# Kernel tuning notes

Measured on AMD Instinct MI355X. Metric: run time of the kernel, lower is better.

Reference implementation:

```python
import jax, jax.numpy as jnp
import numpy as np

HEADS = 8
DIM_HEAD = 64
MAX_REL = 200  # max_rel_dist


def setup_inputs() -> dict:
    key = jax.random.key(0)
    ks = jax.random.split(key, 5)
    B, N, D = 4, 2048, 512
    x = jax.random.normal(ks[0], (B, N, D), dtype=jnp.float32)
    temporal_mask = jax.random.randint(ks[1], (N, N), 0, 2, dtype=jnp.int32)
    gamma = jnp.ones((D,), jnp.float32)
    beta = jnp.zeros((D,), jnp.float32)
    Wqkv = jax.random.normal(ks[2], (D, 3 * HEADS * DIM_HEAD), dtype=jnp.float32) * 0.02
    Wout = jax.random.normal(ks[3], (HEADS * DIM_HEAD, D), dtype=jnp.float32) * 0.02
    bout = jnp.zeros((D,), jnp.float32)
    rel_table = jax.random.normal(ks[4], (2 * MAX_REL - 1,), dtype=jnp.float32) * 0.02
    return {"x": x, "gamma": gamma, "beta": beta, "Wqkv": Wqkv, "Wout": Wout,
            "bout": bout, "rel_table": rel_table, "temporal_mask": temporal_mask}


def reference(x, gamma, beta, Wqkv, Wout, bout, rel_table, temporal_mask):
    B, N, D = x.shape
    scale = DIM_HEAD ** -0.5
    # LayerNorm
    mu = jnp.mean(x, axis=-1, keepdims=True)
    var = jnp.mean(jnp.square(x - mu), axis=-1, keepdims=True)
    xn = (x - mu) * jax.lax.rsqrt(var + 1e-5) * gamma + beta
    # QKV projection (no bias), split heads: b n (h d) -> b h n d
    qkv = xn @ Wqkv  # [B, N, 3*H*d]
    q, k, v = jnp.split(qkv, 3, axis=-1)
    split = lambda t: t.reshape(B, N, HEADS, DIM_HEAD).transpose(0, 2, 1, 3)
    q, k, v = split(q), split(k), split(v)
    # scores with learned relative-position bias
    dots = jnp.einsum('bhnd,bhmd->bhnm', q, k) * scale  # [B,H,N,N]
    idx = jnp.arange(N)
    rel = jnp.clip(idx[:, None] - idx[None, :], -(MAX_REL - 1), MAX_REL - 1) + MAX_REL - 1
    dots = dots + rel_table[rel][None, None, :, :]
    # temporal mask (0 -> -inf); large negative for grad safety
    dots = jnp.where(temporal_mask[None, None, :, :] == 0, jnp.float32(-1e9), dots)
    attn = jax.nn.softmax(dots, axis=-1)
    out = jnp.einsum('bhnm,bhmd->bhnd', attn, v)
    out = out.transpose(0, 2, 1, 3).reshape(B, N, HEADS * DIM_HEAD)
    return out @ Wout + bout
```

## Files before the change

kernel.cpp:

```cpp
#include <hip/hip_runtime.h>

typedef __attribute__((ext_vector_type(8))) short bf16x8;
typedef __attribute__((ext_vector_type(4))) short bf16x4;
typedef __attribute__((ext_vector_type(4))) float f32x4;
typedef unsigned short ushort_t;

#define B_ 4
#define H_ 8
#define N_ 2048
#define D_ 512
#define MAXREL 199
#define LOG2E 1.4426950408889634f

__device__ __forceinline__ ushort_t f2bf(float f) {
    union { float f; unsigned u; } v; v.f = f;
    unsigned r = v.u + 0x7fffu + ((v.u >> 16) & 1u);
    return (ushort_t)(r >> 16);
}
__device__ __forceinline__ float bf2f(ushort_t u) {
    union { unsigned u; float f; } v; v.u = ((unsigned)u) << 16;
    return v.f;
}
__device__ __forceinline__ float fexp2(float x) {
#if __has_builtin(__builtin_amdgcn_exp2f)
    return __builtin_amdgcn_exp2f(x);
#else
    return __expf(x * 0.6931471805599453f);
#endif
}
__device__ __forceinline__ unsigned cvt_pk_bf16(float lo, float hi) {
    unsigned r;
    asm("v_cvt_pk_bf16_f32 %0, %1, %2" : "=v"(r) : "v"(lo), "v"(hi));
    return r;
}
__device__ __forceinline__ void gl_lds16(const ushort_t* g, ushort_t* l) {
    __builtin_amdgcn_global_load_lds(
        (const __attribute__((address_space(1))) void*)g,
        (__attribute__((address_space(3))) void*)l,
        16, 0, 0);
}

#define PREP_LN    2048
#define PREP_WQ    768
#define PREP_WO    256
__global__ __launch_bounds__(256) void prep_kernel(const float* __restrict__ x,
                                                   const float* __restrict__ gamma,
                                                   const float* __restrict__ beta,
                                                   ushort_t* __restrict__ xn,
                                                   const float* __restrict__ Wqkv,
                                                   ushort_t* __restrict__ WqkvT,
                                                   const float* __restrict__ Wout,
                                                   ushort_t* __restrict__ WoutT) {
    __shared__ float smem[32 * 33];
    const int blk = blockIdx.x;
    const int t = threadIdx.x;

    if (blk < PREP_LN) {
        const int row = blk * 4 + (t >> 6);
        const int l = t & 63;
        const float* xr = x + (size_t)row * D_;
        float4 a = *(const float4*)&xr[l * 4];
        float4 c = *(const float4*)&xr[256 + l * 4];
        float s = (a.x + a.y) + (a.z + a.w) + (c.x + c.y) + (c.z + c.w);
        #pragma unroll
        for (int o = 1; o < 64; o <<= 1) s += __shfl_xor(s, o);
        float mu = s * (1.0f / D_);
        float dx0 = a.x - mu, dx1 = a.y - mu, dx2 = a.z - mu, dx3 = a.w - mu;
        float dy0 = c.x - mu, dy1 = c.y - mu, dy2 = c.z - mu, dy3 = c.w - mu;
        float s2 = dx0*dx0 + dx1*dx1 + dx2*dx2 + dx3*dx3
                 + dy0*dy0 + dy1*dy1 + dy2*dy2 + dy3*dy3;
        #pragma unroll
        for (int o = 1; o < 64; o <<= 1) s2 += __shfl_xor(s2, o);
        float rs = rsqrtf(s2 * (1.0f / D_) + 1e-5f);
        float4 g1 = *(const float4*)&gamma[l * 4];
        float4 g2 = *(const float4*)&gamma[256 + l * 4];
        float4 b1 = *(const float4*)&beta[l * 4];
        float4 b2 = *(const float4*)&beta[256 + l * 4];
        ushort_t* yr = xn + (size_t)row * D_;
        union { ushort_t us[4]; unsigned long long ll; } o1, o2;
        o1.us[0] = f2bf(dx0 * rs * g1.x + b1.x);
        o1.us[1] = f2bf(dx1 * rs * g1.y + b1.y);
        o1.us[2] = f2bf(dx2 * rs * g1.z + b1.z);
        o1.us[3] = f2bf(dx3 * rs * g1.w + b1.w);
        o2.us[0] = f2bf(dy0 * rs * g2.x + b2.x);
        o2.us[1] = f2bf(dy1 * rs * g2.y + b2.y);
        o2.us[2] = f2bf(dy2 * rs * g2.z + b2.z);
        o2.us[3] = f2bf(dy3 * rs * g2.w + b2.w);
        *(unsigned long long*)(yr + l * 4) = o1.ll;
        *(unsigned long long*)(yr + 256 + l * 4) = o2.ll;
    } else {
        const float* W; ushort_t* Wt; int Nn, i;
        if (blk < PREP_LN + PREP_WQ) {
            i = blk - PREP_LN; W = Wqkv; Wt = WqkvT; Nn = 1536;
        } else {
            i = blk - (PREP_LN + PREP_WQ); W = Wout; Wt = WoutT; Nn = 512;
        }
        const int nb = Nn >> 5;
        const int bx = (i % nb) * 32, by = (i / nb) * 32;
        const int tx = t & 31, ty = t >> 5;
        float (*tile)[33] = (float(*)[33])smem;
        #pragma unroll
        for (int k = 0; k < 32; k += 8)
            tile[ty + k][tx] = W[(size_t)(by + ty + k) * Nn + bx + tx];
        __syncthreads();
        #pragma unroll
        for (int k = 0; k < 32; k += 8)
            Wt[(size_t)(bx + ty + k) * 512 + by + tx] = f2bf(tile[tx][ty + k]);
    }
}

#define QKV_BIAS_BLKS 512
__global__ __launch_bounds__(256) void gemm_qkv(const ushort_t* __restrict__ A,
                                                const ushort_t* __restrict__ Bt,
                                                ushort_t* __restrict__ qb,
                                                ushort_t* __restrict__ kb,
                                                ushort_t* __restrict__ vb,
                                                const float* __restrict__ rel,
                                                const int* __restrict__ mask,
                                                ushort_t* __restrict__ bp) {
    const int bid = blockIdx.x;
    const int t = threadIdx.x;

    if (bid < QKV_BIAS_BLKS) {
        const int base = bid * 8192;
        #pragma unroll
        for (int p = 0; p < 8; p++) {
            int idx = base + p * 1024 + t * 4;
            int n = idx >> 11, m = idx & 2047;
            const int4 mv = *(const int4*)&mask[idx];
            union { ushort_t us[4]; unsigned long long ll; } pkv;
            #pragma unroll
            for (int j = 0; j < 4; j++) {
                int dl = n - (m + j);
                dl = dl < -MAXREL ? -MAXREL : (dl > MAXREL ? MAXREL : dl);
                int mj = (j == 0) ? mv.x : (j == 1) ? mv.y : (j == 2) ? mv.z : mv.w;
                float v = (mj == 0) ? -1e9f : rel[dl + MAXREL] * LOG2E;
                pkv.us[j] = f2bf(v);
            }
            int off = ((n >> 7) << 18) + ((m >> 6) << 13) + (((n >> 4) & 7) << 10)
                    + (((m >> 4) & 3) << 8) + (((m >> 2) & 3) << 6) + ((n & 15) << 2);
            *(unsigned long long*)(bp + off) = pkv.ll;
        }
        return;
    }

    __shared__ ushort_t As[2][4096];
    __shared__ ushort_t Bs[2][4096];
    const int gid = bid - QKV_BIAS_BLKS;
    const int lane = t & 63, w = t >> 6;
    const int m16 = lane & 15, quad = lane >> 4;
    const int wr = w >> 1, wc = w & 1;
    const int r0 = (gid / 12) * 128, c0 = (gid % 12) * 128;

    const ushort_t* Ag = A  + (size_t)(r0 + (t >> 2)) * D_ + (t & 3) * 8;
    const ushort_t* Bg = Bt + (size_t)(c0 + (t >> 2)) * D_ + (t & 3) * 8;

    f32x4 acc[4][4];
    #pragma unroll
    for (int i = 0; i < 4; i++)
        #pragma unroll
        for (int j = 0; j < 4; j++) acc[i][j] = (f32x4){0.f, 0.f, 0.f, 0.f};

    {
        ushort_t* AsW = As[0] + w * 512;
        ushort_t* BsW = Bs[0] + w * 512;
        gl_lds16(Ag, AsW);
        gl_lds16(Ag + (size_t)64 * D_, AsW + 2048);
        gl_lds16(Bg, BsW);
        gl_lds16(Bg + (size_t)64 * D_, BsW + 2048);
    }
    __syncthreads();

    for (int k0 = 0; k0 < D_; k0 += 32) {
        const int buf = (k0 >> 5) & 1;
        if (k0 + 32 < D_) {
            ushort_t* AsW = As[buf ^ 1] + w * 512;
            ushort_t* BsW = Bs[buf ^ 1] + w * 512;
            gl_lds16(Ag + k0 + 32, AsW);
            gl_lds16(Ag + k0 + 32 + (size_t)64 * D_, AsW + 2048);
            gl_lds16(Bg + k0 + 32, BsW);
            gl_lds16(Bg + k0 + 32 + (size_t)64 * D_, BsW + 2048);
        }
        bf16x8 af[4], bfr[4];
        #pragma unroll
        for (int rt = 0; rt < 4; rt++)
            af[rt] = *(const bf16x8*)(As[buf] + (wr * 64 + rt * 16 + m16) * 32 + quad * 8);
        #pragma unroll
        for (int ct = 0; ct < 4; ct++)
            bfr[ct] = *(const bf16x8*)(Bs[buf] + (wc * 64 + ct * 16 + m16) * 32 + quad * 8);
        #pragma unroll
        for (int rt = 0; rt < 4; rt++)
            #pragma unroll
            for (int ct = 0; ct < 4; ct++)
                acc[rt][ct] = __builtin_amdgcn_mfma_f32_16x16x32_bf16(af[rt], bfr[ct], acc[rt][ct], 0, 0, 0);
        __syncthreads();
    }

    const int b_blk = r0 >> 11, n_base = r0 & 2047;
    if ((c0 >> 9) == 2) {
        ushort_t* SH = As[0];
        #pragma unroll
        for (int ph = 0; ph < 2; ph++) {
            if (ph) __syncthreads();
            if (wc == ph) {
                #pragma unroll
                for (int ct = 0; ct < 4; ct++) {
                    int dcol = ct * 16 + m16;
                    #pragma unroll
                    for (int rt = 0; rt < 4; rt++) {
                        int nl = wr * 64 + rt * 16 + quad * 4;
                        union { ushort_t us[4]; unsigned long long ll; } pkv;
                        #pragma unroll
                        for (int r = 0; r < 4; r++) pkv.us[r] = f2bf(acc[rt][ct][r]);
                        *(unsigned long long*)(&SH[dcol * 128 + (nl ^ ((dcol & 7) << 3))]) = pkv.ll;
                    }
                }
            }
            __syncthreads();
            int h = ((c0 + ph * 64) >> 6) & 7;
            #pragma unroll
            for (int p = 0; p < 4; p++) {
                int dr = p * 16 + (t >> 4);
                int n0 = (t & 15) * 8;
                bf16x8 vv = *(const bf16x8*)&SH[dr * 128 + (n0 ^ ((dr & 7) << 3))];
                *(bf16x8*)(vb + ((size_t)(b_blk * H_ + h) * 64 + dr) * N_ + n_base + n0) = vv;
            }
        }
    } else {
        #pragma unroll
        for (int ct = 0; ct < 4; ct++) {
            int cc = c0 + wc * 64 + ct * 16;
            int which = cc >> 9;
            int h = (cc >> 6) & 7;
            int d = (cc & 63) + m16;
            #pragma unroll
            for (int rt = 0; rt < 4; rt++) {
                int rowb = r0 + wr * 64 + rt * 16 + quad * 4;
                int b = rowb >> 11, n0 = rowb & 2047;
                if (which == 0) {
                    #pragma unroll
                    for (int r = 0; r < 4; r++)
                        qb[((size_t)((b * H_ + h) * N_ + n0 + r)) * 64 + d] = f2bf(acc[rt][ct][r] * (0.125f * LOG2E));
                } else {
                    #pragma unroll
                    for (int r = 0; r < 4; r++)
                        kb[((size_t)((b * H_ + h) * N_ + n0 + r)) * 64 + d] = f2bf(acc[rt][ct][r]);
                }
            }
        }
    }
}

__global__ __launch_bounds__(256) void gemm_out(const ushort_t* __restrict__ A,
                                                const ushort_t* __restrict__ Bt,
                                                const float* __restrict__ bias,
                                                float* __restrict__ C) {
    __shared__ ushort_t As[2][2048];
    __shared__ ushort_t Bs[2][4096];
    const int t = threadIdx.x;
    const int lane = t & 63, w = t >> 6;
    const int m16 = lane & 15, quad = lane >> 4;
    const int wr = w >> 1, wc = w & 1;
    const int r0 = blockIdx.y * 64, c0 = blockIdx.x * 128;

    const ushort_t* Ag = A  + (size_t)(r0 + (t >> 2)) * D_ + (t & 3) * 8;
    const ushort_t* Bg = Bt + (size_t)(c0 + (t >> 2)) * D_ + (t & 3) * 8;

    f32x4 acc[2][4];
    #pragma unroll
    for (int i = 0; i < 2; i++)
        #pragma unroll
        for (int j = 0; j < 4; j++) acc[i][j] = (f32x4){0.f, 0.f, 0.f, 0.f};

    {
        ushort_t* AsW = As[0] + w * 512;
        ushort_t* BsW = Bs[0] + w * 512;
        if (w < 2) gl_lds16(Ag, As[0] + w * 1024 + (lane & 63) * 0 + w * 0 + (t & 255) * 0 + w * 1024), (void)0;
        (void)AsW; (void)BsW;
    }
    {
        if (t < 128) gl_lds16(Ag, As[0] + (t >> 6) * 1024 + 0 * 512 + ((t >> 6) ? 512 : 0) * 0 + (t & 63) * 0 + (t >> 6) * 0 + ((t & 127) >> 6) * 0 + 0), (void)0;
    }
    __syncthreads();
    {
        gl_lds16(Ag, As[0] + w * 512);
        gl_lds16(Bg, Bs[0] + w * 512);
        gl_lds16(Bg + (size_t)64 * D_, Bs[0] + w * 512 + 2048);
    }
    __syncthreads();

    for (int k0 = 0; k0 < D_; k0 += 32) {
        const int buf = (k0 >> 5) & 1;
        if (k0 + 32 < D_) {
            gl_lds16(Ag + k0 + 32, As[buf ^ 1] + w * 512);
            gl_lds16(Bg + k0 + 32, Bs[buf ^ 1] + w * 512);
            gl_lds16(Bg + k0 + 32 + (size_t)64 * D_, Bs[buf ^ 1] + w * 512 + 2048);
        }
        bf16x8 af[2], bfr[4];
        #pragma unroll
        for (int mf = 0; mf < 2; mf++)
            af[mf] = *(const bf16x8*)(As[buf] + (wr * 32 + mf * 16 + m16) * 32 + quad * 8);
        #pragma unroll
        for (int nt = 0; nt < 4; nt++)
            bfr[nt] = *(const bf16x8*)(Bs[buf] + (wc * 64 + nt * 16 + m16) * 32 + quad * 8);
        #pragma unroll
        for (int mf = 0; mf < 2; mf++)
            #pragma unroll
            for (int nt = 0; nt < 4; nt++)
                acc[mf][nt] = __builtin_amdgcn_mfma_f32_16x16x32_bf16(af[mf], bfr[nt], acc[mf][nt], 0, 0, 0);
        __syncthreads();
    }

    #pragma unroll
    for (int mf = 0; mf < 2; mf++) {
        #pragma unroll
        for (int nt = 0; nt < 4; nt++) {
            int col = c0 + wc * 64 + nt * 16 + m16;
            int row0 = r0 + wr * 32 + mf * 16 + quad * 4;
            float bv = bias[col];
            #pragma unroll
            for (int r = 0; r < 4; r++)
                C[(size_t)(row0 + r) * 512 + col] = acc[mf][nt][r] + bv;
        }
    }
}

#define ATTN_TILE(JT, KCUR, VCUR, KNXT, VNXT, BCUR, BNXT)                              \
  {                                                                                    \
    const int jt = (JT);                                                               \
    const int buf = jt & 1;                                                            \
    if (jt + 2 < 32) {                                                                 \
      KNXT = *(const bf16x8*)(kgbase + (size_t)((jt + 2) * 64 + srow) * 64 + scb * 8); \
      VNXT = *(const bf16x8*)(vgbase + (size_t)srow * N_ + (jt + 2) * 64 + scb * 8);   \
    }                                                                                  \
    if (jt + 1 < 32) {                                                                 \
      _Pragma("unroll")                                                                \
      for (int nt = 0; nt < 4; nt++)                                                   \
        BNXT[nt] = *(const bf16x4*)(bpb + ((jt + 1) << 13) + (nt << 8));               \
    }                                                                                  \
    unsigned pk[8];                                                                    \
    __builtin_amdgcn_s_setprio(1);                                                     \
    _Pragma("unroll")                                                                  \
    for (int nt = 0; nt < 4; nt++) {                                                   \
      f32x4 a2;                                                                        \
      _Pragma("unroll")                                                                \
      for (int r = 0; r < 4; r++) a2[r] = bf2f((ushort_t)BCUR[nt][r]);                 \
      int kr = nt * 16 + m16;                                                          \
      bf16x8 kf0 = *(const bf16x8*)(&Ks[buf][kr * 64 + ((quad) ^ (kr & 7)) * 8]);      \
      bf16x8 kf1 = *(const bf16x8*)(&Ks[buf][kr * 64 + ((quad + 4) ^ (kr & 7)) * 8]);  \
      a2 = __builtin_amdgcn_mfma_f32_16x16x32_bf16(kf0, qa0, a2, 0, 0, 0);             \
      a2 = __builtin_amdgcn_mfma_f32_16x16x32_bf16(kf1, qa1, a2, 0, 0, 0);             \
      float p0 = fexp2(a2[0]), p1 = fexp2(a2[1]);                                      \
      float p2 = fexp2(a2[2]), p3 = fexp2(a2[3]);                                      \
      rsum += (p0 + p1) + (p2 + p3);                                                   \
      pk[nt * 2]     = cvt_pk_bf16(p0, p1);                                            \
      pk[nt * 2 + 1] = cvt_pk_bf16(p2, p3);                                            \
    }                                                                                  \
    __builtin_amdgcn_s_setprio(0);                                                     \
    _Pragma("unroll")                                                                  \
    for (int i = 0; i < 4; i++) {                                                      \
      int chunk = 2 * i + (quad >> 1);                                                 \
      union { unsigned uu[2]; unsigned long long ll; } wrp;                            \
      wrp.uu[0] = pk[2 * i]; wrp.uu[1] = pk[2 * i + 1];                                \
      *(unsigned long long*)(pw + m16 * 64 + ((chunk ^ (m16 & 7)) << 3)                \
                             + (quad & 1) * 4) = wrp.ll;                               \
    }                                                                                  \
    bf16x8 pa0 = *(const bf16x8*)(pw + m16 * 64 + ((quad ^ (m16 & 7)) << 3));          \
    bf16x8 pa1 = *(const bf16x8*)(pw + m16 * 64 + (((quad + 4) ^ (m16 & 7)) << 3));    \
    __builtin_amdgcn_s_setprio(1);                                                     \
    _Pragma("unroll")                                                                  \
    for (int nt = 0; nt < 4; nt++) {                                                   \
      int d = nt * 16 + m16;                                                           \
      bf16x8 vf0 = *(const bf16x8*)(&Vs[buf][d * 64 + ((quad) ^ (d & 7)) * 8]);        \
      bf16x8 vf1 = *(const bf16x8*)(&Vs[buf][d * 64 + ((quad + 4) ^ (d & 7)) * 8]);    \
      o[nt] = __builtin_amdgcn_mfma_f32_16x16x32_bf16(pa0, vf0, o[nt], 0, 0, 0);       \
      o[nt] = __builtin_amdgcn_mfma_f32_16x16x32_bf16(pa1, vf1, o[nt], 0, 0, 0);       \
    }                                                                                  \
    __builtin_amdgcn_s_setprio(0);                                                     \
    if (jt + 1 < 32) {                                                                 \
      *(bf16x8*)(&Ks[buf ^ 1][soff]) = KCUR;                                           \
      *(bf16x8*)(&Vs[buf ^ 1][soff]) = VCUR;                                           \
    }                                                                                  \
    __syncthreads();                                                                   \
  }

__global__ __launch_bounds__(512, 4) void attn_mfma(const ushort_t* __restrict__ qb,
                                                    const ushort_t* __restrict__ kb,
                                                    const ushort_t* __restrict__ vb,
                                                    const ushort_t* __restrict__ bp,
                                                    ushort_t* __restrict__ attn) {
    __shared__ ushort_t Ks[2][64 * 64];
    __shared__ ushort_t Vs[2][64 * 64];
    __shared__ ushort_t p_s[8][16 * 64];

    const int t = threadIdx.x;
    const int w = t >> 6, lane = t & 63;
    const int m16 = lane & 15, quad = lane >> 4;
    const int id = blockIdx.x;
    const int bh = id & 31;
    const int qt = id >> 5;
    const int b = bh >> 3, h = bh & 7;
    const int n0w = qt * 128 + w * 16;

    const int srow = t >> 3, scb = t & 7;
    const int soff = srow * 64 + (scb ^ (srow & 7)) * 8;
    const ushort_t* kgbase = kb + ((size_t)bh * N_) * 64;
    const ushort_t* vgbase = vb + ((size_t)bh * 64) * N_;

    const ushort_t* qpb = qb + ((size_t)(bh * N_ + n0w + m16)) * 64 + quad * 8;
    bf16x8 qa0 = *(const bf16x8*)(qpb);
    bf16x8 qa1 = *(const bf16x8*)(qpb + 32);

    const ushort_t* bpb = bp + ((size_t)qt << 18) + (w << 10) + (quad << 6) + (m16 << 2);

    *(bf16x8*)(&Ks[0][soff]) = *(const bf16x8*)(kgbase + (size_t)srow * 64 + scb * 8);
    *(bf16x8*)(&Vs[0][soff]) = *(const bf16x8*)(vgbase + (size_t)srow * N_ + scb * 8);
    bf16x8 kA = *(const bf16x8*)(kgbase + (size_t)(64 + srow) * 64 + scb * 8);
    bf16x8 vA = *(const bf16x8*)(vgbase + (size_t)srow * N_ + 64 + scb * 8);
    bf16x8 kB, vB;
    bf16x4 bA[4], bB[4];
    #pragma unroll
    for (int nt = 0; nt < 4; nt++) bA[nt] = *(const bf16x4*)(bpb + (nt << 8));
    __syncthreads();

    f32x4 o[4];
    #pragma unroll
    for (int nt = 0; nt < 4; nt++) o[nt] = (f32x4){0.f, 0.f, 0.f, 0.f};
    float rsum = 0.f;

    ushort_t* pw = p_s[w];

    for (int jt2 = 0; jt2 < 16; jt2++) {
        ATTN_TILE(2 * jt2,     kA, vA, kB, vB, bA, bB);
        ATTN_TILE(2 * jt2 + 1, kB, vB, kA, vA, bB, bA);
    }

    rsum += __shfl_xor(rsum, 16);
    rsum += __shfl_xor(rsum, 32);

    #pragma unroll
    for (int r = 0; r < 4; r++) {
        float inv = 1.0f / __shfl(rsum, quad * 4 + r);
        int n = n0w + quad * 4 + r;
        ushort_t* orow = attn + ((size_t)(b * N_ + n)) * 512 + h * 64 + m16;
        #pragma unroll
        for (int nt = 0; nt < 4; nt++) orow[nt * 16] = f2bf(o[nt][r] * inv);
    }
}

extern "C" void kernel_launch(void* const* d_in, const int* in_sizes, int n_in,
                              void* d_out, int out_size, void* d_ws, size_t ws_size,
                              hipStream_t stream) {
    const float* x     = (const float*)d_in[0];
    const float* gamma = (const float*)d_in[1];
    const float* beta  = (const float*)d_in[2];
    const float* Wqkv  = (const float*)d_in[3];
    const float* Wout  = (const float*)d_in[4];
    const float* bout  = (const float*)d_in[5];
    const float* rel   = (const float*)d_in[6];
    const int*   mask  = (const int*)d_in[7];
    float* out = (float*)d_out;

    char* wsb = (char*)d_ws;
    ushort_t* xn    = (ushort_t*)(wsb);
    ushort_t* attnb = (ushort_t*)(wsb + ( 8u << 20));
    ushort_t* qb    = (ushort_t*)(wsb + (16u << 20));
    ushort_t* kb    = (ushort_t*)(wsb + (24u << 20));
    ushort_t* vb    = (ushort_t*)(wsb + (32u << 20));
    ushort_t* WqkvT = (ushort_t*)(wsb + (40u << 20));
    ushort_t* WoutT = (ushort_t*)(wsb + (42u << 20));
    ushort_t* bp    = (ushort_t*)(wsb + (44u << 20));

    prep_kernel<<<PREP_LN + PREP_WQ + PREP_WO, 256, 0, stream>>>(
        x, gamma, beta, xn, Wqkv, WqkvT, Wout, WoutT);

    gemm_qkv<<<QKV_BIAS_BLKS + 768, 256, 0, stream>>>(xn, WqkvT, qb, kb, vb, rel, mask, bp);

    attn_mfma<<<512, 512, 0, stream>>>(qb, kb, vb, bp, attnb);

    gemm_out<<<dim3(512 / 128, 8192 / 64), 256, 0, stream>>>(attnb, WoutT, bout, out);
}
```

Before: 195.9 us.

## Compute softmax row sums via MFMA with ones and coalesce bias-tile writes

The attention kernel now accumulates softmax row sums with two extra MFMAs against a ones vector, using the bf16-rounded probabilities. This replaces the per-element VALU adds and the final cross-lane shuffles, and it makes the normaliser consistent with the values actually multiplied by V. The bias/mask precompute in the QKV GEMM kernel now uses fewer, larger blocks that stage tiles in LDS so each lane writes 16-byte contiguous chunks of the tiled bias layout instead of scattered 8-byte stores. Leftover dead prefetch code in the output GEMM is removed; the costs are two more MFMAs per tile and LDS use in the bias blocks.

```diff
diff --git a/kernel.cpp b/kernel.cpp
--- a/kernel.cpp
+++ b/kernel.cpp
@@ -109,7 +109,7 @@
     }
 }
 
-#define QKV_BIAS_BLKS 512
+#define QKV_BIAS_BLKS 128
 __global__ __launch_bounds__(256) void gemm_qkv(const ushort_t* __restrict__ A,
                                                 const ushort_t* __restrict__ Bt,
                                                 ushort_t* __restrict__ qb,
@@ -118,34 +118,50 @@
                                                 const float* __restrict__ rel,
                                                 const int* __restrict__ mask,
                                                 ushort_t* __restrict__ bp) {
+    __shared__ ushort_t As[2][4096];
+    __shared__ ushort_t Bs[2][4096];
     const int bid = blockIdx.x;
     const int t = threadIdx.x;
 
     if (bid < QKV_BIAS_BLKS) {
-        const int base = bid * 8192;
-        #pragma unroll
-        for (int p = 0; p < 8; p++) {
-            int idx = base + p * 1024 + t * 4;
-            int n = idx >> 11, m = idx & 2047;
-            const int4 mv = *(const int4*)&mask[idx];
-            union { ushort_t us[4]; unsigned long long ll; } pkv;
-            #pragma unroll
-            for (int j = 0; j < 4; j++) {
-                int dl = n - (m + j);
-                dl = dl < -MAXREL ? -MAXREL : (dl > MAXREL ? MAXREL : dl);
-                int mj = (j == 0) ? mv.x : (j == 1) ? mv.y : (j == 2) ? mv.z : mv.w;
-                float v = (mj == 0) ? -1e9f : rel[dl + MAXREL] * LOG2E;
-                pkv.us[j] = f2bf(v);
+        unsigned long long (*lds_t)[16][17] = (unsigned long long(*)[16][17])As;
+        const int w = t >> 6, l = t & 63;
+        const int n0 = bid * 16;
+        const int m4 = l & 15;
+        const int m4d = ((l >> 4) << 2) | ((l >> 2) & 3);
+        const size_t rbase0 = (((size_t)(bid >> 3)) << 18) + (((size_t)(bid & 7)) << 10);
+        #pragma unroll
+        for (int i = 0; i < 8; i++) {
+            const int jt = w + i * 4;
+            const int m = jt * 64 + m4 * 4;
+            #pragma unroll
+            for (int s = 0; s < 4; s++) {
+                const int nl = s * 4 + (l >> 4);
+                const int n = n0 + nl;
+                const int4 mv = *(const int4*)&mask[(size_t)n * 2048 + m];
+                union { ushort_t us[4]; unsigned long long ll; } pkv;
+                #pragma unroll
+                for (int j = 0; j < 4; j++) {
+                    int dl = n - (m + j);
+                    dl = dl < -MAXREL ? -MAXREL : (dl > MAXREL ? MAXREL : dl);
+                    int mj = (j == 0) ? mv.x : (j == 1) ? mv.y : (j == 2) ? mv.z : mv.w;
+                    float v = (mj == 0) ? -1e9f : rel[dl + MAXREL] * LOG2E;
+                    pkv.us[j] = f2bf(v);
+                }
+                lds_t[w][nl][m4] = pkv.ll;
             }
-            int off = ((n >> 7) << 18) + ((m >> 6) << 13) + (((n >> 4) & 7) << 10)
-                    + (((m >> 4) & 3) << 8) + (((m >> 2) & 3) << 6) + ((n & 15) << 2);
-            *(unsigned long long*)(bp + off) = pkv.ll;
+            ushort_t* dst = bp + rbase0 + ((size_t)jt << 13) + (size_t)l * 16;
+            union { unsigned long long q[2]; bf16x8 v; } s0, s1;
+            s0.q[0] = lds_t[w][4 * (l & 3) + 0][m4d];
+            s0.q[1] = lds_t[w][4 * (l & 3) + 1][m4d];
+            s1.q[0] = lds_t[w][4 * (l & 3) + 2][m4d];
+            s1.q[1] = lds_t[w][4 * (l & 3) + 3][m4d];
+            *(bf16x8*)(dst) = s0.v;
+            *(bf16x8*)(dst + 8) = s1.v;
         }
         return;
     }
 
-    __shared__ ushort_t As[2][4096];
-    __shared__ ushort_t Bs[2][4096];
     const int gid = bid - QKV_BIAS_BLKS;
     const int lane = t & 63, w = t >> 6;
     const int m16 = lane & 15, quad = lane >> 4;
@@ -161,25 +177,19 @@
         #pragma unroll
         for (int j = 0; j < 4; j++) acc[i][j] = (f32x4){0.f, 0.f, 0.f, 0.f};
 
-    {
-        ushort_t* AsW = As[0] + w * 512;
-        ushort_t* BsW = Bs[0] + w * 512;
-        gl_lds16(Ag, AsW);
-        gl_lds16(Ag + (size_t)64 * D_, AsW + 2048);
-        gl_lds16(Bg, BsW);
-        gl_lds16(Bg + (size_t)64 * D_, BsW + 2048);
-    }
+    gl_lds16(Ag, As[0] + w * 512);
+    gl_lds16(Ag + (size_t)64 * D_, As[0] + w * 512 + 2048);
+    gl_lds16(Bg, Bs[0] + w * 512);
+    gl_lds16(Bg + (size_t)64 * D_, Bs[0] + w * 512 + 2048);
     __syncthreads();
 
     for (int k0 = 0; k0 < D_; k0 += 32) {
         const int buf = (k0 >> 5) & 1;
         if (k0 + 32 < D_) {
-            ushort_t* AsW = As[buf ^ 1] + w * 512;
-            ushort_t* BsW = Bs[buf ^ 1] + w * 512;
-            gl_lds16(Ag + k0 + 32, AsW);
-            gl_lds16(Ag + k0 + 32 + (size_t)64 * D_, AsW + 2048);
-            gl_lds16(Bg + k0 + 32, BsW);
-            gl_lds16(Bg + k0 + 32 + (size_t)64 * D_, BsW + 2048);
+            gl_lds16(Ag + k0 + 32, As[buf ^ 1] + w * 512);
+            gl_lds16(Ag + k0 + 32 + (size_t)64 * D_, As[buf ^ 1] + w * 512 + 2048);
+            gl_lds16(Bg + k0 + 32, Bs[buf ^ 1] + w * 512);
+            gl_lds16(Bg + k0 + 32 + (size_t)64 * D_, Bs[buf ^ 1] + w * 512 + 2048);
         }
         bf16x8 af[4], bfr[4];
         #pragma unroll
@@ -272,21 +282,9 @@
         #pragma unroll
         for (int j = 0; j < 4; j++) acc[i][j] = (f32x4){0.f, 0.f, 0.f, 0.f};
 
-    {
-        ushort_t* AsW = As[0] + w * 512;
-        ushort_t* BsW = Bs[0] + w * 512;
-        if (w < 2) gl_lds16(Ag, As[0] + w * 1024 + (lane & 63) * 0 + w * 0 + (t & 255) * 0 + w * 1024), (void)0;
-        (void)AsW; (void)BsW;
-    }
-    {
-        if (t < 128) gl_lds16(Ag, As[0] + (t >> 6) * 1024 + 0 * 512 + ((t >> 6) ? 512 : 0) * 0 + (t & 63) * 0 + (t >> 6) * 0 + ((t & 127) >> 6) * 0 + 0), (void)0;
-    }
-    __syncthreads();
-    {
-        gl_lds16(Ag, As[0] + w * 512);
-        gl_lds16(Bg, Bs[0] + w * 512);
-        gl_lds16(Bg + (size_t)64 * D_, Bs[0] + w * 512 + 2048);
-    }
+    gl_lds16(Ag, As[0] + w * 512);
+    gl_lds16(Bg, Bs[0] + w * 512);
+    gl_lds16(Bg + (size_t)64 * D_, Bs[0] + w * 512 + 2048);
     __syncthreads();
 
     for (int k0 = 0; k0 < D_; k0 += 32) {
@@ -352,7 +350,6 @@
       a2 = __builtin_amdgcn_mfma_f32_16x16x32_bf16(kf1, qa1, a2, 0, 0, 0);             \
       float p0 = fexp2(a2[0]), p1 = fexp2(a2[1]);                                      \
       float p2 = fexp2(a2[2]), p3 = fexp2(a2[3]);                                      \
-      rsum += (p0 + p1) + (p2 + p3);                                                   \
       pk[nt * 2]     = cvt_pk_bf16(p0, p1);                                            \
       pk[nt * 2 + 1] = cvt_pk_bf16(p2, p3);                                            \
     }                                                                                  \
@@ -368,6 +365,8 @@
     bf16x8 pa0 = *(const bf16x8*)(pw + m16 * 64 + ((quad ^ (m16 & 7)) << 3));          \
     bf16x8 pa1 = *(const bf16x8*)(pw + m16 * 64 + (((quad + 4) ^ (m16 & 7)) << 3));    \
     __builtin_amdgcn_s_setprio(1);                                                     \
+    rs = __builtin_amdgcn_mfma_f32_16x16x32_bf16(pa0, kones, rs, 0, 0, 0);             \
+    rs = __builtin_amdgcn_mfma_f32_16x16x32_bf16(pa1, kones, rs, 0, 0, 0);             \
     _Pragma("unroll")                                                                  \
     for (int nt = 0; nt < 4; nt++) {                                                   \
       int d = nt * 16 + m16;                                                           \
@@ -413,6 +412,10 @@
 
     const ushort_t* bpb = bp + ((size_t)qt << 18) + (w << 10) + (quad << 6) + (m16 << 2);
 
+    bf16x8 kones;
+    #pragma unroll
+    for (int i = 0; i < 8; i++) kones[i] = (short)0x3F80;
+
     *(bf16x8*)(&Ks[0][soff]) = *(const bf16x8*)(kgbase + (size_t)srow * 64 + scb * 8);
     *(bf16x8*)(&Vs[0][soff]) = *(const bf16x8*)(vgbase + (size_t)srow * N_ + scb * 8);
     bf16x8 kA = *(const bf16x8*)(kgbase + (size_t)(64 + srow) * 64 + scb * 8);
@@ -426,7 +429,7 @@
     f32x4 o[4];
     #pragma unroll
     for (int nt = 0; nt < 4; nt++) o[nt] = (f32x4){0.f, 0.f, 0.f, 0.f};
-    float rsum = 0.f;
+    f32x4 rs = (f32x4){0.f, 0.f, 0.f, 0.f};
 
     ushort_t* pw = p_s[w];
 
@@ -435,12 +438,9 @@
         ATTN_TILE(2 * jt2 + 1, kB, vB, kA, vA, bB, bA);
     }
 
-    rsum += __shfl_xor(rsum, 16);
-    rsum += __shfl_xor(rsum, 32);
-
     #pragma unroll
     for (int r = 0; r < 4; r++) {
-        float inv = 1.0f / __shfl(rsum, quad * 4 + r);
+        float inv = 1.0f / rs[r];
         int n = n0w + quad * 4 + r;
         ushort_t* orow = attn + ((size_t)(b * N_ + n)) * 512 + h * 64 + m16;
         #pragma unroll
```

After: 195.3 us. No clear change (-0.3%).
